# Kernel optimization log

Measured on AMD Instinct MI355X. Metric: run time of the kernel, lower is better.

Reference implementation:

```python
import jax, jax.numpy as jnp
import numpy as np

N = 30000      # nodes
E = 480000     # edges (before self loops)
DIN = 128      # dim_in
DH = 32        # dim_h (per-head out channels)
H1 = 8         # gat1 heads
H2 = 2         # gat2 heads
G = 64         # num graphs in batch
DOUT = 10      # dim_out
NEG_SLOPE = 0.2


def _glorot(key, shape):
    fan_in = shape[0]
    return jax.random.normal(key, shape, dtype=jnp.float32) / np.sqrt(fan_in)


def setup_inputs() -> dict:
    key = jax.random.key(0)
    ks = jax.random.split(key, 16)
    x = jax.random.normal(ks[0], (N, DIN), dtype=jnp.float32)
    edge_index = jax.random.randint(ks[1], (2, E), 0, N, dtype=jnp.int32)
    batch = jnp.sort(jax.random.randint(ks[2], (N,), 0, G, dtype=jnp.int32))
    # GATv2Conv layer 1: lin_l, lin_r (dim_in -> H1*DH), att (H1, DH), bias (H1*DH)
    W1l = _glorot(ks[3], (DIN, H1 * DH))
    W1r = _glorot(ks[4], (DIN, H1 * DH))
    a1 = _glorot(ks[5], (DH, H1)).T  # [H1, DH]
    b1 = jnp.zeros((H1 * DH,), dtype=jnp.float32)
    # GATv2Conv layer 2: (H1*DH -> H2*DH)
    W2l = _glorot(ks[6], (H1 * DH, H2 * DH))
    W2r = _glorot(ks[7], (H1 * DH, H2 * DH))
    a2 = _glorot(ks[8], (DH, H2)).T  # [H2, DH]
    b2 = jnp.zeros((H2 * DH,), dtype=jnp.float32)
    # MLP head: fc1(2*DH -> DH), fc2(DH -> DH//2), fc(DH//2 -> DOUT); stored [in,out]
    fc1_w = _glorot(ks[9], (2 * DH, DH)); fc1_b = jnp.zeros((DH,), jnp.float32)
    fc2_w = _glorot(ks[10], (DH, DH // 2)); fc2_b = jnp.zeros((DH // 2,), jnp.float32)
    fc_w = _glorot(ks[11], (DH // 2, DOUT)); fc_b = jnp.zeros((DOUT,), jnp.float32)
    return {"x": x, "edge_index": edge_index, "batch": batch,
            "W1l": W1l, "W1r": W1r, "a1": a1, "b1": b1,
            "W2l": W2l, "W2r": W2r, "a2": a2, "b2": b2,
            "fc1_w": fc1_w, "fc1_b": fc1_b, "fc2_w": fc2_w, "fc2_b": fc2_b,
            "fc_w": fc_w, "fc_b": fc_b}


def gatv2_conv(x, edge_index, Wl, Wr, att, bias, heads, dh, n):
    """PyG GATv2Conv: concat=True, add_self_loops=True, negative_slope=0.2."""
    src, dst = edge_index[0], edge_index[1]
    loop = jnp.arange(n, dtype=src.dtype)        # self loops (PyG default)
    src = jnp.concatenate([src, loop])
    dst = jnp.concatenate([dst, loop])
    xl = (x @ Wl).reshape(n, heads, dh)          # source transform
    xr = (x @ Wr).reshape(n, heads, dh)          # destination transform
    xj = xl[src]                                  # [Etot, H, dh] message features
    s = jax.nn.leaky_relu(xj + xr[dst], NEG_SLOPE)
    e = jnp.einsum('ehd,hd->eh', s, att)          # per-edge per-head score
    # segment softmax over incoming edges of each destination node
    m = jax.ops.segment_max(e, dst, num_segments=n)
    p = jnp.exp(e - m[dst])
    z = jax.ops.segment_sum(p, dst, num_segments=n)
    alpha = p / z[dst]                            # [Etot, H]
    out = jax.ops.segment_sum(xj * alpha[..., None], dst, num_segments=n)
    return out.reshape(n, heads * dh) + bias


def reference(x, edge_index, batch, W1l, W1r, a1, b1, W2l, W2r, a2, b2,
              fc1_w, fc1_b, fc2_w, fc2_b, fc_w, fc_b):
    h = gatv2_conv(x, edge_index, W1l, W1r, a1, b1, H1, DH, N)
    h = jax.nn.elu(h)
    h = gatv2_conv(h, edge_index, W2l, W2r, a2, b2, H2, DH, N)  # [N, 2*DH]
    # global_mean_pool
    sums = jax.ops.segment_sum(h, batch, num_segments=G)
    cnt = jax.ops.segment_sum(jnp.ones((N,), h.dtype), batch, num_segments=G)
    hg = sums / jnp.maximum(cnt, 1.0)[:, None]    # [G, 2*DH]
    x1 = jax.nn.relu(hg @ fc1_w + fc1_b)
    # dropout p=0.2 is identity in eval mode
    x2 = jax.nn.relu(x1 @ fc2_w + fc2_b)
    c = x2 @ fc_w + fc_b
    return (c, x2)
```

## Files before the change

### kernel.cpp

```cpp
#include <hip/hip_runtime.h>
#include <math.h>

#define DIN 128
#define DH  32
#define H1  8
#define H2  2
#define GNUM 64
#define DOUT 10
#define NEG_SLOPE 0.2f
#define SCAN_B 512

typedef __attribute__((ext_vector_type(8))) short sv8;
typedef __attribute__((ext_vector_type(4))) float fv4;

static __device__ __forceinline__ unsigned short f2bf(float f) {
    unsigned int u = __float_as_uint(f);
    unsigned int r = (u + 0x7fffu + ((u >> 16) & 1u)) >> 16;
    return (unsigned short)r;
}
static __device__ __forceinline__ float bf2f(unsigned short h) {
    return __uint_as_float(((unsigned int)h) << 16);
}


__global__ void k_prep(const float* __restrict__ x,
                       const float* __restrict__ W1l, const float* __restrict__ W1r,
                       const float* __restrict__ W2l, const float* __restrict__ W2r,
                       unsigned short* __restrict__ xgh, unsigned short* __restrict__ xgl,
                       short* __restrict__ B1th, short* __restrict__ B1tl,
                       short* __restrict__ B2th, short* __restrict__ B2tl,
                       int* __restrict__ zbase, int nz, int n) {
    int id = blockIdx.x * blockDim.x + threadIdx.x;
    if (id < nz) zbase[id] = 0;
    const int NX = n * 32;
    const int T1 = 512 * 128;
    const int T2 = 128 * 256;
    if (id < NX) {
        int m = id >> 5, j4 = id & 31;
        float4 v = *(const float4*)(x + (size_t)m * 128 + j4 * 4);
        unsigned short hx = f2bf(v.x), hy = f2bf(v.y), hz = f2bf(v.z), hw = f2bf(v.w);
        ushort4 hi; hi.x = hx; hi.y = hy; hi.z = hz; hi.w = hw;
        ushort4 lo;
        lo.x = f2bf(v.x - bf2f(hx)); lo.y = f2bf(v.y - bf2f(hy));
        lo.z = f2bf(v.z - bf2f(hz)); lo.w = f2bf(v.w - bf2f(hw));
        int R = m >> 4, r = m & 15;
        int C = j4 >> 3, q = (j4 >> 1) & 3, j = (j4 & 1) * 4;
        size_t o = ((size_t)(R * 4 + C) * 64 + q * 16 + r) * 8 + j;
        *(ushort4*)(xgh + o) = hi;
        *(ushort4*)(xgl + o) = lo;
    } else if (id < NX + T1) {
        int id1 = id - NX;
        int nn = id1 / 128, k = id1 - nn * 128;
        float v = (nn < 256) ? W1l[(size_t)k * 256 + nn] : W1r[(size_t)k * 256 + (nn - 256)];
        unsigned short h = f2bf(v);
        size_t o = (((size_t)(nn >> 4) * 4 + (k >> 5)) * 64 + ((k >> 3) & 3) * 16 + (nn & 15)) * 8 + (k & 7);
        B1th[o] = (short)h;
        B1tl[o] = (short)f2bf(v - bf2f(h));
    } else if (id < NX + T1 + T2) {
        int id2 = id - NX - T1;
        int nn = id2 / 256, k = id2 - nn * 256;
        float v = (nn < 64) ? W2l[(size_t)k * 64 + nn] : W2r[(size_t)k * 64 + (nn - 64)];
        unsigned short h = f2bf(v);
        size_t o = (((size_t)(nn >> 4) * 8 + (k >> 5)) * 64 + ((k >> 3) & 3) * 16 + (nn & 15)) * 8 + (k & 7);
        B2th[o] = (short)h;
        B2tl[o] = (short)f2bf(v - bf2f(h));
    }
}

__global__ void k_deg(const int* __restrict__ dst, int* __restrict__ deg, int E, int n) {
    int i = blockIdx.x * blockDim.x + threadIdx.x;
    if (i < E) {
        atomicAdd(&deg[dst[i]], 1);
    } else if (i < E + n) {
        atomicAdd(&deg[i - E], 1);
    }
}

__global__ __launch_bounds__(SCAN_B)
void k_scan_partial(const int* __restrict__ deg, int* __restrict__ bsum, int n) {
    int i = blockIdx.x * SCAN_B + threadIdx.x;
    int v = (i < n) ? deg[i] : 0;
    #pragma unroll
    for (int m = 32; m >= 1; m >>= 1) v += __shfl_xor(v, m);
    __shared__ int red[SCAN_B / 64];
    if ((threadIdx.x & 63) == 0) red[threadIdx.x >> 6] = v;
    __syncthreads();
    if (threadIdx.x == 0) {
        int s = 0;
        #pragma unroll
        for (int k = 0; k < SCAN_B / 64; ++k) s += red[k];
        bsum[blockIdx.x] = s;
    }
}

__global__ __launch_bounds__(SCAN_B)
void k_scan_apply(int* __restrict__ deg, int* __restrict__ cursor,
                  const int* __restrict__ bsum, int n, int nb) {
    __shared__ int buf[SCAN_B];
    __shared__ int pfx_s, tot_s;
    const int t = threadIdx.x, b = blockIdx.x;
    if (t < 64) {
        int v = (t < nb) ? bsum[t] : 0;
        int incl = v;
        #pragma unroll
        for (int o = 1; o < 64; o <<= 1) {
            int w = __shfl_up(incl, o);
            if (t >= o) incl += w;
        }
        int pfx = (b == 0) ? 0 : __shfl(incl, b - 1);
        int tot = __shfl(incl, nb - 1);
        if (t == 0) { pfx_s = pfx; tot_s = tot; }
    }
    int i = b * SCAN_B + t;
    int v = (i < n) ? deg[i] : 0;
    buf[t] = v;
    __syncthreads();
    for (int o = 1; o < SCAN_B; o <<= 1) {
        int a = (t >= o) ? buf[t - o] : 0;
        __syncthreads();
        buf[t] += a;
        __syncthreads();
    }
    int excl = buf[t] - v + pfx_s;
    if (i < n) { deg[i] = excl; cursor[i] = excl; }
    if (b == 0 && t == 0) deg[n] = tot_s;
}

__global__ void k_scatter(const int* __restrict__ src, const int* __restrict__ dst,
                          int* __restrict__ cursor, int* __restrict__ csr_src, int E, int n) {
    int i = blockIdx.x * blockDim.x + threadIdx.x;
    if (i < E) {
        int d = dst[i];
        int pos = atomicAdd(&cursor[d], 1);
        csr_src[pos] = src[i];
    } else if (i < E + n) {
        int v = i - E;
        int pos = atomicAdd(&cursor[v], 1);
        csr_src[pos] = v;
    }
}

__global__ __launch_bounds__(256, 2)
void k_gemm1(const unsigned short* __restrict__ Ah, const unsigned short* __restrict__ Al,
             const short* __restrict__ Bth, const short* __restrict__ Btl,
             unsigned short* __restrict__ C,
             int M, int Ntot) {
    __shared__ float smc[64 * 68];
    const int tid = threadIdx.x;
    const int lane = tid & 63;
    const int wid = tid >> 6;
    const int wm = wid & 1, wn = wid >> 1;
    const int m0 = blockIdx.x * 128;
    const int n0 = blockIdx.y * 128;
    const int l15 = lane & 15, q = lane >> 4;
    const int MR = (M >> 4) - 1;

    fv4 acc[4][4] = {};

    const unsigned short* ap[4];
    const unsigned short* alp[4];
    #pragma unroll
    for (int fm = 0; fm < 4; ++fm) {
        int R = (m0 >> 4) + wm * 4 + fm;
        if (R > MR) R = MR;
        ap[fm]  = Ah + ((size_t)R * 4 * 64 + lane) * 8;
        alp[fm] = Al + ((size_t)R * 4 * 64 + lane) * 8;
    }
    const short* bhp[4];
    const short* blp[4];
    #pragma unroll
    for (int fn = 0; fn < 4; ++fn) {
        int R = (n0 >> 4) + wn * 4 + fn;
        bhp[fn] = Bth + ((size_t)R * 4 * 64 + lane) * 8;
        blp[fn] = Btl + ((size_t)R * 4 * 64 + lane) * 8;
    }

    #pragma unroll
    for (int c = 0; c < 4; ++c) {
        const size_t co = (size_t)c * 512;
        sv8 ah[4], al[4], bh[4], bl[4];
        #pragma unroll
        for (int fn = 0; fn < 4; ++fn) {
            bh[fn] = *(const sv8*)(bhp[fn] + co);
            bl[fn] = *(const sv8*)(blp[fn] + co);
        }
        #pragma unroll
        for (int fm = 0; fm < 4; ++fm) {
            ah[fm] = *(const sv8*)(ap[fm] + co);
            al[fm] = *(const sv8*)(alp[fm] + co);
        }
        #pragma unroll
        for (int fm = 0; fm < 4; ++fm) {
            #pragma unroll
            for (int fn = 0; fn < 4; ++fn) {
                acc[fm][fn] = __builtin_amdgcn_mfma_f32_16x16x32_bf16(ah[fm], bh[fn], acc[fm][fn], 0, 0, 0);
                acc[fm][fn] = __builtin_amdgcn_mfma_f32_16x16x32_bf16(ah[fm], bl[fn], acc[fm][fn], 0, 0, 0);
                acc[fm][fn] = __builtin_amdgcn_mfma_f32_16x16x32_bf16(al[fm], bh[fn], acc[fm][fn], 0, 0, 0);
            }
        }
    }

    #pragma unroll
    for (int s = 0; s < 2; ++s) {
        #pragma unroll
        for (int cn = 0; cn < 2; ++cn) {
            __syncthreads();
            if (wm == s && wn == cn) {
                #pragma unroll
                for (int fm = 0; fm < 4; ++fm)
                    #pragma unroll
                    for (int fn = 0; fn < 4; ++fn)
                        #pragma unroll
                        for (int r = 0; r < 4; ++r)
                            smc[(fm * 16 + q * 4 + r) * 68 + fn * 16 + l15] = acc[fm][fn][r];
            }
            __syncthreads();
            int lr = tid >> 2;
            int grow = m0 + s * 64 + lr;
            if (grow < M) {
                #pragma unroll
                for (int k4 = 0; k4 < 4; ++k4) {
                    int jj = (tid & 3) + k4 * 4;
                    float4 vv = *(float4*)&smc[lr * 68 + jj * 4];
                    int gcol = n0 + cn * 64 + jj * 4;
                    ushort4 uu;
                    uu.x = f2bf(vv.x); uu.y = f2bf(vv.y);
                    uu.z = f2bf(vv.z); uu.w = f2bf(vv.w);
                    *(ushort4*)(C + (size_t)grow * Ntot + gcol) = uu;
                }
            }
        }
    }
}

__global__ __launch_bounds__(256, 2)
void k_gemm_bf(const unsigned short* __restrict__ A, const short* __restrict__ Bth,
               const short* __restrict__ Btl,
               unsigned short* __restrict__ C,
               int M, int Ntot) {
    __shared__ float smc[64 * 36];
    const int tid = threadIdx.x;
    const int lane = tid & 63;
    const int wid = tid >> 6;
    const int wm = wid & 1, wn = wid >> 1;
    const int m0 = blockIdx.x * 128;
    const int n0 = blockIdx.y * 64;
    const int l15 = lane & 15, q = lane >> 4;
    const int MR = (M >> 4) - 1;

    fv4 acc[4][2] = {};

    const unsigned short* ap[4];
    #pragma unroll
    for (int fm = 0; fm < 4; ++fm) {
        int R = (m0 >> 4) + wm * 4 + fm;
        if (R > MR) R = MR;
        ap[fm] = A + ((size_t)R * 8 * 64 + lane) * 8;
    }
    const short* bhp[2];
    const short* blp[2];
    #pragma unroll
    for (int fn = 0; fn < 2; ++fn) {
        int R = (n0 >> 4) + wn * 2 + fn;
        bhp[fn] = Bth + ((size_t)R * 8 * 64 + lane) * 8;
        blp[fn] = Btl + ((size_t)R * 8 * 64 + lane) * 8;
    }

    #pragma unroll 4
    for (int c = 0; c < 8; ++c) {
        const size_t co = (size_t)c * 512;
        sv8 ah[4], bh[2], bl[2];
        #pragma unroll
        for (int fn = 0; fn < 2; ++fn) {
            bh[fn] = *(const sv8*)(bhp[fn] + co);
            bl[fn] = *(const sv8*)(blp[fn] + co);
        }
        #pragma unroll
        for (int fm = 0; fm < 4; ++fm)
            ah[fm] = *(const sv8*)(ap[fm] + co);
        #pragma unroll
        for (int fm = 0; fm < 4; ++fm) {
            #pragma unroll
            for (int fn = 0; fn < 2; ++fn) {
                acc[fm][fn] = __builtin_amdgcn_mfma_f32_16x16x32_bf16(ah[fm], bh[fn], acc[fm][fn], 0, 0, 0);
                acc[fm][fn] = __builtin_amdgcn_mfma_f32_16x16x32_bf16(ah[fm], bl[fn], acc[fm][fn], 0, 0, 0);
            }
        }
    }

    #pragma unroll
    for (int s = 0; s < 2; ++s) {
        #pragma unroll
        for (int cn = 0; cn < 2; ++cn) {
            __syncthreads();
            if (wm == s && wn == cn) {
                #pragma unroll
                for (int fm = 0; fm < 4; ++fm)
                    #pragma unroll
                    for (int fn = 0; fn < 2; ++fn)
                        #pragma unroll
                        for (int r = 0; r < 4; ++r)
                            smc[(fm * 16 + q * 4 + r) * 36 + fn * 16 + l15] = acc[fm][fn][r];
            }
            __syncthreads();
            int lr = tid >> 2;
            int grow = m0 + s * 64 + lr;
            if (grow < M) {
                #pragma unroll
                for (int k4 = 0; k4 < 2; ++k4) {
                    int jj = (tid & 3) + k4 * 4;
                    float4 vv = *(float4*)&smc[lr * 36 + jj * 4];
                    int gcol = n0 + cn * 32 + jj * 4;
                    ushort4 uu;
                    uu.x = f2bf(vv.x); uu.y = f2bf(vv.y);
                    uu.z = f2bf(vv.z); uu.w = f2bf(vv.w);
                    *(ushort4*)(C + (size_t)grow * Ntot + gcol) = uu;
                }
            }
        }
    }
}

__global__ __launch_bounds__(64)
void k_edge1(const unsigned short* __restrict__ XLR,
             const int* __restrict__ offs, const int* __restrict__ csr,
             const float* __restrict__ att, const float* __restrict__ bias,
             unsigned short* __restrict__ out, int n) {
    const int lane = threadIdx.x;
    const int v = blockIdx.x;
    const int li = lane & 31;
    const int half = lane >> 5;
    const uint4* XL4 = (const uint4*)XLR;
    float av[8], xr[8];
    #pragma unroll
    for (int k = 0; k < 8; ++k) av[k] = att[li * 8 + k];
    {
        uint4 u = XL4[(size_t)v * 64 + 32 + li];
        xr[0] = __uint_as_float(u.x << 16);  xr[1] = __uint_as_float(u.x & 0xffff0000u);
        xr[2] = __uint_as_float(u.y << 16);  xr[3] = __uint_as_float(u.y & 0xffff0000u);
        xr[4] = __uint_as_float(u.z << 16);  xr[5] = __uint_as_float(u.z & 0xffff0000u);
        xr[6] = __uint_as_float(u.w << 16);  xr[7] = __uint_as_float(u.w & 0xffff0000u);
    }
    float z = 0.f;
    float acc[8] = {};
    const int e0 = offs[v], e1 = offs[v + 1];
    for (int j0 = e0; j0 < e1; j0 += 4) {
        #pragma unroll
        for (int p = 0; p < 2; ++p) {
            int j = j0 + p * 2 + half;
            bool valid = (j < e1);
            int jj = valid ? j : (e1 - 1);
            int src = csr[jj];
            uint4 u = XL4[(size_t)src * 64 + li];
            float f[8];
            f[0] = __uint_as_float(u.x << 16);  f[1] = __uint_as_float(u.x & 0xffff0000u);
            f[2] = __uint_as_float(u.y << 16);  f[3] = __uint_as_float(u.y & 0xffff0000u);
            f[4] = __uint_as_float(u.z << 16);  f[5] = __uint_as_float(u.z & 0xffff0000u);
            f[6] = __uint_as_float(u.w << 16);  f[7] = __uint_as_float(u.w & 0xffff0000u);
            float s1 = 0.f, s2 = 0.f;
            #pragma unroll
            for (int k = 0; k < 8; ++k) {
                float t = f[k] + xr[k];
                s1 = fmaf(t, av[k], s1);
                s2 = fmaf(fabsf(t), av[k], s2);
            }
            float s = fmaf(0.6f, s1, 0.4f * s2);
            s += __shfl_xor(s, 1);
            s += __shfl_xor(s, 2);
            float w = valid ? __expf(s) : 0.f;
            z += w;
            #pragma unroll
            for (int k = 0; k < 8; ++k) acc[k] = fmaf(w, f[k], acc[k]);
        }
    }
    z += __shfl_xor(z, 32);
    #pragma unroll
    for (int k = 0; k < 8; ++k) acc[k] += __shfl_xor(acc[k], 32);
    if (half == 0) {
        const float rz = 1.f / z;
        unsigned int o[4];
        #pragma unroll
        for (int k2 = 0; k2 < 4; ++k2) {
            float lo = fmaf(acc[k2 * 2 + 0], rz, bias[li * 8 + k2 * 2 + 0]);
            float hi = fmaf(acc[k2 * 2 + 1], rz, bias[li * 8 + k2 * 2 + 1]);
            lo = (lo > 0.f) ? lo : (__expf(lo) - 1.f);
            hi = (hi > 0.f) ? hi : (__expf(hi) - 1.f);
            o[k2] = (unsigned int)f2bf(lo) | ((unsigned int)f2bf(hi) << 16);
        }
        uint4 ov = { o[0], o[1], o[2], o[3] };
        size_t po = (((size_t)(v >> 4) * 8 + (li >> 2)) * 64 + (li & 3) * 16 + (v & 15)) * 8;
        *(uint4*)(out + po) = ov;
    }
}

__global__ __launch_bounds__(64)
void k_edge2(const unsigned short* __restrict__ XLR,
             const int* __restrict__ offs, const int* __restrict__ csr,
             const float* __restrict__ att, const float* __restrict__ bias,
             float* __restrict__ out, int n) {
    const int lane = threadIdx.x;
    const int v = blockIdx.x;
    const int li = lane & 7;
    const int slot = lane >> 3;
    const uint4* XL4 = (const uint4*)XLR;
    float av[8], xr[8];
    #pragma unroll
    for (int k = 0; k < 8; ++k) av[k] = att[li * 8 + k];
    {
        uint4 u = XL4[(size_t)v * 16 + 8 + li];
        xr[0] = __uint_as_float(u.x << 16);  xr[1] = __uint_as_float(u.x & 0xffff0000u);
        xr[2] = __uint_as_float(u.y << 16);  xr[3] = __uint_as_float(u.y & 0xffff0000u);
        xr[4] = __uint_as_float(u.z << 16);  xr[5] = __uint_as_float(u.z & 0xffff0000u);
        xr[6] = __uint_as_float(u.w << 16);  xr[7] = __uint_as_float(u.w & 0xffff0000u);
    }
    float z = 0.f;
    float acc[8] = {};
    const int e0 = offs[v], e1 = offs[v + 1];
    for (int j0 = e0; j0 < e1; j0 += 8) {
        int j = j0 + slot;
        bool valid = (j < e1);
        int jj = valid ? j : (e1 - 1);
        int src = csr[jj];
        uint4 u = XL4[(size_t)src * 16 + li];
        float f[8];
        f[0] = __uint_as_float(u.x << 16);  f[1] = __uint_as_float(u.x & 0xffff0000u);
        f[2] = __uint_as_float(u.y << 16);  f[3] = __uint_as_float(u.y & 0xffff0000u);
        f[4] = __uint_as_float(u.z << 16);  f[5] = __uint_as_float(u.z & 0xffff0000u);
        f[6] = __uint_as_float(u.w << 16);  f[7] = __uint_as_float(u.w & 0xffff0000u);
        float s1 = 0.f, s2 = 0.f;
        #pragma unroll
        for (int k = 0; k < 8; ++k) {
            float t = f[k] + xr[k];
            s1 = fmaf(t, av[k], s1);
            s2 = fmaf(fabsf(t), av[k], s2);
        }
        float s = fmaf(0.6f, s1, 0.4f * s2);
        s += __shfl_xor(s, 1);
        s += __shfl_xor(s, 2);
        float w = valid ? __expf(s) : 0.f;
        z += w;
        #pragma unroll
        for (int k = 0; k < 8; ++k) acc[k] = fmaf(w, f[k], acc[k]);
    }
    z += __shfl_xor(z, 8);  z += __shfl_xor(z, 16);  z += __shfl_xor(z, 32);
    #pragma unroll
    for (int k = 0; k < 8; ++k) {
        acc[k] += __shfl_xor(acc[k], 8);
        acc[k] += __shfl_xor(acc[k], 16);
        acc[k] += __shfl_xor(acc[k], 32);
    }
    if (slot == 0) {
        const float rz = 1.f / z;
        float o[8];
        #pragma unroll
        for (int k = 0; k < 8; ++k)
            o[k] = fmaf(acc[k], rz, bias[li * 8 + k]);
        float4 o0 = { o[0], o[1], o[2], o[3] };
        float4 o1 = { o[4], o[5], o[6], o[7] };
        *(float4*)(out + (size_t)v * 64 + li * 8 + 0) = o0;
        *(float4*)(out + (size_t)v * 64 + li * 8 + 4) = o1;
    }
}

__global__ __launch_bounds__(256)
void k_pool_mlp(const float* __restrict__ out2, const int* __restrict__ batch,
                const float* __restrict__ fc1w, const float* __restrict__ fc1b,
                const float* __restrict__ fc2w, const float* __restrict__ fc2b,
                const float* __restrict__ fcw,  const float* __restrict__ fcb,
                float* __restrict__ outc, float* __restrict__ outx2, int n) {
    const int g = blockIdx.x;
    const int t = threadIdx.x;
    const int lane = t & 63;
    const int w = t >> 6;
    __shared__ float red[4][64];
    __shared__ float hg_s[64];
    __shared__ float x1_s[32];
    __shared__ float x2_s[16];

    int lo = 0, hi = n;
    while (lo < hi) { int mid = (lo + hi) >> 1; if (batch[mid] < g) lo = mid + 1; else hi = mid; }
    const int start = lo;
    hi = n;
    while (lo < hi) { int mid = (lo + hi) >> 1; if (batch[mid] < g + 1) lo = mid + 1; else hi = mid; }
    const int end = lo;

    float s = 0.f;
    for (int v = start + w; v < end; v += 4)
        s += out2[(size_t)v * 64 + lane];
    red[w][lane] = s;
    __syncthreads();
    if (w == 0) {
        float tot = red[0][lane] + red[1][lane] + red[2][lane] + red[3][lane];
        float cnt = fmaxf((float)(end - start), 1.0f);
        hg_s[lane] = tot / cnt;
    }
    __syncthreads();
    if (t < 32) {
        float a = fc1b[t];
        #pragma unroll
        for (int k = 0; k < 64; ++k) a = fmaf(hg_s[k], fc1w[k * 32 + t], a);
        x1_s[t] = fmaxf(a, 0.f);
    }
    __syncthreads();
    if (t < 16) {
        float a = fc2b[t];
        #pragma unroll
        for (int k = 0; k < 32; ++k) a = fmaf(x1_s[k], fc2w[k * 16 + t], a);
        x2_s[t] = fmaxf(a, 0.f);
    }
    __syncthreads();
    if (t < DOUT) {
        float a = fcb[t];
        #pragma unroll
        for (int k = 0; k < 16; ++k) a = fmaf(x2_s[k], fcw[k * 10 + t], a);
        outc[g * DOUT + t] = a;
    }
    if (t < 16) outx2[g * 16 + t] = x2_s[t];
}

extern "C" void kernel_launch(void* const* d_in, const int* in_sizes, int n_in,
                              void* d_out, int out_size, void* d_ws, size_t ws_size,
                              hipStream_t stream) {
    const float* x    = (const float*)d_in[0];
    const int*   ei   = (const int*)d_in[1];
    const int*   batch= (const int*)d_in[2];
    const float* W1l  = (const float*)d_in[3];
    const float* W1r  = (const float*)d_in[4];
    const float* a1   = (const float*)d_in[5];
    const float* b1   = (const float*)d_in[6];
    const float* W2l  = (const float*)d_in[7];
    const float* W2r  = (const float*)d_in[8];
    const float* a2   = (const float*)d_in[9];
    const float* b2   = (const float*)d_in[10];
    const float* fc1w = (const float*)d_in[11];
    const float* fc1b = (const float*)d_in[12];
    const float* fc2w = (const float*)d_in[13];
    const float* fc2b = (const float*)d_in[14];
    const float* fcw  = (const float*)d_in[15];
    const float* fcb  = (const float*)d_in[16];

    const int N = in_sizes[2];
    const int E = in_sizes[1] / 2;
    const int ET = E + N;
    const int* esrc = ei;
    const int* edst = ei + E;
    const int NB = (N + SCAN_B - 1) / SCAN_B;

    char* ws = (char*)d_ws;
    size_t off = 0;
    unsigned short* xlr1b = (unsigned short*)(ws + off); off += (size_t)N * 512 * 2;
    unsigned short* h1b  = (unsigned short*)(ws + off);  off += (size_t)N * 256 * 2;
    float* out2 = (float*)(ws + off);            off += (size_t)N * 64 * 4;
    int*   deg   = (int*)(ws + off);             off += ((size_t)(N + 1) * 4 + 255) & ~255ull;
    int*   cursor= (int*)(ws + off);             off += ((size_t)N * 4 + 255) & ~255ull;
    int*   csr   = (int*)(ws + off);             off += ((size_t)ET * 4 + 255) & ~255ull;
    int*   bsum  = (int*)(ws + off);             off += ((size_t)(NB + 1) * 4 + 255) & ~255ull;
    short* B1th  = (short*)(ws + off);           off += (size_t)512 * 128 * 2;
    short* B1tl  = (short*)(ws + off);           off += (size_t)512 * 128 * 2;
    short* B2th  = (short*)(ws + off);           off += (size_t)128 * 256 * 2;
    short* B2tl  = (short*)(ws + off);           off += (size_t)128 * 256 * 2;
    unsigned short* xgh = (unsigned short*)(ws + off); off += (size_t)N * 128 * 2;
    unsigned short* xgl = (unsigned short*)(ws + off); off += (size_t)N * 128 * 2;
    unsigned short* xlr2b = xlr1b;
    (void)ws_size; (void)n_in; (void)out_size;

    float* outc  = (float*)d_out;
    float* outx2 = (float*)d_out + GNUM * DOUT;

    const int prep_tot = N * 32 + 512 * 128 + 128 * 256;
    k_prep<<<(prep_tot + 255) / 256, 256, 0, stream>>>(
        x, W1l, W1r, W2l, W2r, xgh, xgl, B1th, B1tl, B2th, B2tl, deg, N + 1, N);

    int tb = 256;
    int gb = (ET + tb - 1) / tb;
    k_deg<<<gb, tb, 0, stream>>>(edst, deg, E, N);
    k_scan_partial<<<NB, SCAN_B, 0, stream>>>(deg, bsum, N);
    k_scan_apply<<<NB, SCAN_B, 0, stream>>>(deg, cursor, bsum, N, NB);
    k_scatter<<<gb, tb, 0, stream>>>(esrc, edst, cursor, csr, E, N);

    dim3 g1((N + 127) / 128, 4);
    k_gemm1<<<g1, 256, 0, stream>>>(xgh, xgl, B1th, B1tl, xlr1b, N, 512);

    k_edge1<<<N, 64, 0, stream>>>(xlr1b, deg, csr, a1, b1, h1b, N);

    dim3 g2((N + 127) / 128, 2);
    k_gemm_bf<<<g2, 256, 0, stream>>>(h1b, B2th, B2tl, xlr2b, N, 128);

    k_edge2<<<N, 64, 0, stream>>>(xlr2b, deg, csr, a2, b2, out2, N);

    k_pool_mlp<<<GNUM, 256, 0, stream>>>(out2, batch, fc1w, fc1b, fc2w, fc2b,
                                         fcw, fcb, outc, outx2, N);
}
```

Baseline: 282.2 us.

## Prefetch next neighbor row in edge kernels and pack four nodes per block

Both edge-aggregation kernels now software-pipeline the neighbor gather: the next edge's CSR index and feature row are loaded before the current edge is processed, hiding gather latency. Blocks grow from 64 to 256 threads and each wave handles one destination node, cutting the block count by four and launch/scheduling overhead. In k_edge1 the two-way manual unroll is replaced by a single-edge-per-iteration loop with a prefetch, which can reduce memory-level parallelism per wave and adds register pressure from the extra in-flight row.

```diff
diff --git a/kernel.cpp b/kernel.cpp
--- a/kernel.cpp
+++ b/kernel.cpp
@@ -321,13 +321,15 @@
     }
 }
 
-__global__ __launch_bounds__(64)
+__global__ __launch_bounds__(256)
 void k_edge1(const unsigned short* __restrict__ XLR,
              const int* __restrict__ offs, const int* __restrict__ csr,
              const float* __restrict__ att, const float* __restrict__ bias,
              unsigned short* __restrict__ out, int n) {
-    const int lane = threadIdx.x;
-    const int v = blockIdx.x;
+    const int tid = threadIdx.x;
+    const int lane = tid & 63;
+    const int v = blockIdx.x * 4 + (tid >> 6);
+    if (v >= n) return;
     const int li = lane & 31;
     const int half = lane >> 5;
     const uint4* XL4 = (const uint4*)XLR;
@@ -344,34 +346,41 @@
     float z = 0.f;
     float acc[8] = {};
     const int e0 = offs[v], e1 = offs[v + 1];
-    for (int j0 = e0; j0 < e1; j0 += 4) {
-        #pragma unroll
-        for (int p = 0; p < 2; ++p) {
-            int j = j0 + p * 2 + half;
-            bool valid = (j < e1);
-            int jj = valid ? j : (e1 - 1);
-            int src = csr[jj];
-            uint4 u = XL4[(size_t)src * 64 + li];
-            float f[8];
-            f[0] = __uint_as_float(u.x << 16);  f[1] = __uint_as_float(u.x & 0xffff0000u);
-            f[2] = __uint_as_float(u.y << 16);  f[3] = __uint_as_float(u.y & 0xffff0000u);
-            f[4] = __uint_as_float(u.z << 16);  f[5] = __uint_as_float(u.z & 0xffff0000u);
-            f[6] = __uint_as_float(u.w << 16);  f[7] = __uint_as_float(u.w & 0xffff0000u);
-            float s1 = 0.f, s2 = 0.f;
-            #pragma unroll
-            for (int k = 0; k < 8; ++k) {
-                float t = f[k] + xr[k];
-                s1 = fmaf(t, av[k], s1);
-                s2 = fmaf(fabsf(t), av[k], s2);
-            }
-            float s = fmaf(0.6f, s1, 0.4f * s2);
-            s += __shfl_xor(s, 1);
-            s += __shfl_xor(s, 2);
-            float w = valid ? __expf(s) : 0.f;
-            z += w;
-            #pragma unroll
-            for (int k = 0; k < 8; ++k) acc[k] = fmaf(w, f[k], acc[k]);
-        }
+
+    int j = e0 + half;
+    bool val = (j < e1);
+    int jj = val ? j : (e1 - 1);
+    int src = csr[jj];
+    uint4 u = XL4[(size_t)src * 64 + li];
+
+    for (int base = e0; base < e1; base += 2) {
+        int jn = j + 2;
+        bool valn = (jn < e1);
+        int jjn = valn ? jn : (e1 - 1);
+        int srcn = csr[jjn];
+        uint4 un = XL4[(size_t)srcn * 64 + li];
+
+        float f[8];
+        f[0] = __uint_as_float(u.x << 16);  f[1] = __uint_as_float(u.x & 0xffff0000u);
+        f[2] = __uint_as_float(u.y << 16);  f[3] = __uint_as_float(u.y & 0xffff0000u);
+        f[4] = __uint_as_float(u.z << 16);  f[5] = __uint_as_float(u.z & 0xffff0000u);
+        f[6] = __uint_as_float(u.w << 16);  f[7] = __uint_as_float(u.w & 0xffff0000u);
+        float s1 = 0.f, s2 = 0.f;
+        #pragma unroll
+        for (int k = 0; k < 8; ++k) {
+            float t = f[k] + xr[k];
+            s1 = fmaf(t, av[k], s1);
+            s2 = fmaf(fabsf(t), av[k], s2);
+        }
+        float s = fmaf(0.6f, s1, 0.4f * s2);
+        s += __shfl_xor(s, 1);
+        s += __shfl_xor(s, 2);
+        float w = val ? __expf(s) : 0.f;
+        z += w;
+        #pragma unroll
+        for (int k = 0; k < 8; ++k) acc[k] = fmaf(w, f[k], acc[k]);
+
+        u = un; val = valn; j = jn;
     }
     z += __shfl_xor(z, 32);
     #pragma unroll
@@ -393,13 +402,15 @@
     }
 }
 
-__global__ __launch_bounds__(64)
+__global__ __launch_bounds__(256)
 void k_edge2(const unsigned short* __restrict__ XLR,
              const int* __restrict__ offs, const int* __restrict__ csr,
              const float* __restrict__ att, const float* __restrict__ bias,
              float* __restrict__ out, int n) {
-    const int lane = threadIdx.x;
-    const int v = blockIdx.x;
+    const int tid = threadIdx.x;
+    const int lane = tid & 63;
+    const int v = blockIdx.x * 4 + (tid >> 6);
+    if (v >= n) return;
     const int li = lane & 7;
     const int slot = lane >> 3;
     const uint4* XL4 = (const uint4*)XLR;
@@ -416,12 +427,20 @@
     float z = 0.f;
     float acc[8] = {};
     const int e0 = offs[v], e1 = offs[v + 1];
-    for (int j0 = e0; j0 < e1; j0 += 8) {
-        int j = j0 + slot;
-        bool valid = (j < e1);
-        int jj = valid ? j : (e1 - 1);
-        int src = csr[jj];
-        uint4 u = XL4[(size_t)src * 16 + li];
+
+    int j = e0 + slot;
+    bool val = (j < e1);
+    int jj = val ? j : (e1 - 1);
+    int src = csr[jj];
+    uint4 u = XL4[(size_t)src * 16 + li];
+
+    for (int base = e0; base < e1; base += 8) {
+        int jn = j + 8;
+        bool valn = (jn < e1);
+        int jjn = valn ? jn : (e1 - 1);
+        int srcn = csr[jjn];
+        uint4 un = XL4[(size_t)srcn * 16 + li];
+
         float f[8];
         f[0] = __uint_as_float(u.x << 16);  f[1] = __uint_as_float(u.x & 0xffff0000u);
         f[2] = __uint_as_float(u.y << 16);  f[3] = __uint_as_float(u.y & 0xffff0000u);
@@ -437,10 +456,12 @@
         float s = fmaf(0.6f, s1, 0.4f * s2);
         s += __shfl_xor(s, 1);
         s += __shfl_xor(s, 2);
-        float w = valid ? __expf(s) : 0.f;
+        float w = val ? __expf(s) : 0.f;
         z += w;
         #pragma unroll
         for (int k = 0; k < 8; ++k) acc[k] = fmaf(w, f[k], acc[k]);
+
+        u = un; val = valn; j = jn;
     }
     z += __shfl_xor(z, 8);  z += __shfl_xor(z, 16);  z += __shfl_xor(z, 32);
     #pragma unroll
@@ -581,12 +602,12 @@
     dim3 g1((N + 127) / 128, 4);
     k_gemm1<<<g1, 256, 0, stream>>>(xgh, xgl, B1th, B1tl, xlr1b, N, 512);
 
-    k_edge1<<<N, 64, 0, stream>>>(xlr1b, deg, csr, a1, b1, h1b, N);
+    k_edge1<<<(N + 3) / 4, 256, 0, stream>>>(xlr1b, deg, csr, a1, b1, h1b, N);
 
     dim3 g2((N + 127) / 128, 2);
     k_gemm_bf<<<g2, 256, 0, stream>>>(h1b, B2th, B2tl, xlr2b, N, 128);
 
-    k_edge2<<<N, 64, 0, stream>>>(xlr2b, deg, csr, a2, b2, out2, N);
+    k_edge2<<<(N + 3) / 4, 256, 0, stream>>>(xlr2b, deg, csr, a2, b2, out2, N);
 
     k_pool_mlp<<<GNUM, 256, 0, stream>>>(out2, batch, fc1w, fc1b, fc2w, fc2b,
                                          fcw, fcb, outc, outx2, N);
```

Result: faster. 275.2 us (-2.5%).

## Split XL/XR buffers, persistent atomic-queue edge kernels, packed bf16 epilogue

Applied to the files above, without the earlier changes.

The GEMM outputs are split into separate, contiguous XL and XR arrays, so each gathered source row in the edge kernels covers half as many bytes per row stride and packs more densely in cache. The edge kernels become persistent 256-thread blocks that pull destination nodes from an atomic counter, replacing one 64-thread block per node and hoisting the att and bias loads out of the per-node path. The GEMM epilogues now drain both warp rows at once through a larger LDS tile with fewer barriers, and use the hardware v_cvt_pk_bf16_f32 pack with 16-byte stores. In exchange, every node costs one global atomic, and the larger LDS tile may lower GEMM occupancy.

```diff
diff --git a/kernel.cpp b/kernel.cpp
--- a/kernel.cpp
+++ b/kernel.cpp
@@ -21,6 +21,11 @@
 static __device__ __forceinline__ float bf2f(unsigned short h) {
     return __uint_as_float(((unsigned int)h) << 16);
 }
+static __device__ __forceinline__ unsigned int cvtpk(float lo, float hi) {
+    unsigned int r;
+    asm("v_cvt_pk_bf16_f32 %0, %1, %2" : "=v"(r) : "v"(lo), "v"(hi));
+    return r;
+}
 
 
 __global__ void k_prep(const float* __restrict__ x,
@@ -29,9 +34,10 @@
                        unsigned short* __restrict__ xgh, unsigned short* __restrict__ xgl,
                        short* __restrict__ B1th, short* __restrict__ B1tl,
                        short* __restrict__ B2th, short* __restrict__ B2tl,
-                       int* __restrict__ zbase, int nz, int n) {
+                       int* __restrict__ zbase, int nz, int* __restrict__ ctr, int n) {
     int id = blockIdx.x * blockDim.x + threadIdx.x;
     if (id < nz) zbase[id] = 0;
+    if (id < 2) ctr[id] = 0;
     const int NX = n * 32;
     const int T1 = 512 * 128;
     const int T2 = 128 * 256;
@@ -143,9 +149,9 @@
 __global__ __launch_bounds__(256, 2)
 void k_gemm1(const unsigned short* __restrict__ Ah, const unsigned short* __restrict__ Al,
              const short* __restrict__ Bth, const short* __restrict__ Btl,
-             unsigned short* __restrict__ C,
-             int M, int Ntot) {
-    __shared__ float smc[64 * 68];
+             unsigned short* __restrict__ XLo, unsigned short* __restrict__ XRo,
+             int M) {
+    __shared__ float smc[128 * 68];
     const int tid = threadIdx.x;
     const int lane = tid & 63;
     const int wid = tid >> 6;
@@ -201,33 +207,33 @@
     }
 
     #pragma unroll
-    for (int s = 0; s < 2; ++s) {
-        #pragma unroll
-        for (int cn = 0; cn < 2; ++cn) {
-            __syncthreads();
-            if (wm == s && wn == cn) {
+    for (int p = 0; p < 2; ++p) {
+        if (p) __syncthreads();
+        if (wn == p) {
+            #pragma unroll
+            for (int fm = 0; fm < 4; ++fm)
                 #pragma unroll
-                for (int fm = 0; fm < 4; ++fm)
+                for (int fn = 0; fn < 4; ++fn)
                     #pragma unroll
-                    for (int fn = 0; fn < 4; ++fn)
-                        #pragma unroll
-                        for (int r = 0; r < 4; ++r)
-                            smc[(fm * 16 + q * 4 + r) * 68 + fn * 16 + l15] = acc[fm][fn][r];
-            }
-            __syncthreads();
-            int lr = tid >> 2;
-            int grow = m0 + s * 64 + lr;
-            if (grow < M) {
-                #pragma unroll
-                for (int k4 = 0; k4 < 4; ++k4) {
-                    int jj = (tid & 3) + k4 * 4;
-                    float4 vv = *(float4*)&smc[lr * 68 + jj * 4];
-                    int gcol = n0 + cn * 64 + jj * 4;
-                    ushort4 uu;
-                    uu.x = f2bf(vv.x); uu.y = f2bf(vv.y);
-                    uu.z = f2bf(vv.z); uu.w = f2bf(vv.w);
-                    *(ushort4*)(C + (size_t)grow * Ntot + gcol) = uu;
-                }
+                    for (int r = 0; r < 4; ++r)
+                        smc[(wm * 64 + fm * 16 + q * 4 + r) * 68 + fn * 16 + l15] = acc[fm][fn][r];
+        }
+        __syncthreads();
+        int lr = tid >> 1;
+        int ch = (tid & 1) * 32;
+        int grow = m0 + lr;
+        if (grow < M) {
+            int colb = n0 + p * 64 + ch;
+            unsigned short* dst = (colb < 256)
+                ? XLo + (size_t)grow * 256 + colb
+                : XRo + (size_t)grow * 256 + (colb - 256);
+            #pragma unroll
+            for (int j = 0; j < 4; ++j) {
+                float4 a = *(float4*)&smc[lr * 68 + ch + j * 8];
+                float4 b = *(float4*)&smc[lr * 68 + ch + j * 8 + 4];
+                uint4 o = { cvtpk(a.x, a.y), cvtpk(a.z, a.w),
+                            cvtpk(b.x, b.y), cvtpk(b.z, b.w) };
+                *(uint4*)(dst + j * 8) = o;
             }
         }
     }
@@ -236,9 +242,9 @@
 __global__ __launch_bounds__(256, 2)
 void k_gemm_bf(const unsigned short* __restrict__ A, const short* __restrict__ Bth,
                const short* __restrict__ Btl,
-               unsigned short* __restrict__ C,
-               int M, int Ntot) {
-    __shared__ float smc[64 * 36];
+               unsigned short* __restrict__ XL2, unsigned short* __restrict__ XR2,
+               int M) {
+    __shared__ float smc[128 * 36];
     const int tid = threadIdx.x;
     const int lane = tid & 63;
     const int wid = tid >> 6;
@@ -289,69 +295,156 @@
     }
 
     #pragma unroll
-    for (int s = 0; s < 2; ++s) {
-        #pragma unroll
-        for (int cn = 0; cn < 2; ++cn) {
-            __syncthreads();
-            if (wm == s && wn == cn) {
+    for (int p = 0; p < 2; ++p) {
+        if (p) __syncthreads();
+        if (wn == p) {
+            #pragma unroll
+            for (int fm = 0; fm < 4; ++fm)
                 #pragma unroll
-                for (int fm = 0; fm < 4; ++fm)
+                for (int fn = 0; fn < 2; ++fn)
                     #pragma unroll
-                    for (int fn = 0; fn < 2; ++fn)
-                        #pragma unroll
-                        for (int r = 0; r < 4; ++r)
-                            smc[(fm * 16 + q * 4 + r) * 36 + fn * 16 + l15] = acc[fm][fn][r];
+                    for (int r = 0; r < 4; ++r)
+                        smc[(wm * 64 + fm * 16 + q * 4 + r) * 36 + fn * 16 + l15] = acc[fm][fn][r];
+        }
+        __syncthreads();
+        int lr = tid >> 1;
+        int ch = (tid & 1) * 16;
+        int grow = m0 + lr;
+        if (grow < M) {
+            int colb = n0 + p * 32 + ch;
+            unsigned short* dst = (colb < 64)
+                ? XL2 + (size_t)grow * 64 + colb
+                : XR2 + (size_t)grow * 64 + (colb - 64);
+            #pragma unroll
+            for (int j = 0; j < 2; ++j) {
+                float4 a = *(float4*)&smc[lr * 36 + ch + j * 8];
+                float4 b = *(float4*)&smc[lr * 36 + ch + j * 8 + 4];
+                uint4 o = { cvtpk(a.x, a.y), cvtpk(a.z, a.w),
+                            cvtpk(b.x, b.y), cvtpk(b.z, b.w) };
+                *(uint4*)(dst + j * 8) = o;
             }
-            __syncthreads();
-            int lr = tid >> 2;
-            int grow = m0 + s * 64 + lr;
-            if (grow < M) {
-                #pragma unroll
-                for (int k4 = 0; k4 < 2; ++k4) {
-                    int jj = (tid & 3) + k4 * 4;
-                    float4 vv = *(float4*)&smc[lr * 36 + jj * 4];
-                    int gcol = n0 + cn * 32 + jj * 4;
-                    ushort4 uu;
-                    uu.x = f2bf(vv.x); uu.y = f2bf(vv.y);
-                    uu.z = f2bf(vv.z); uu.w = f2bf(vv.w);
-                    *(ushort4*)(C + (size_t)grow * Ntot + gcol) = uu;
-                }
-            }
-        }
-    }
-}
-
-__global__ __launch_bounds__(64)
-void k_edge1(const unsigned short* __restrict__ XLR,
+        }
+    }
+}
+
+__global__ __launch_bounds__(256)
+void k_edge1(const unsigned short* __restrict__ XL, const unsigned short* __restrict__ XR,
              const int* __restrict__ offs, const int* __restrict__ csr,
              const float* __restrict__ att, const float* __restrict__ bias,
-             unsigned short* __restrict__ out, int n) {
-    const int lane = threadIdx.x;
-    const int v = blockIdx.x;
+             unsigned short* __restrict__ out, int* __restrict__ ctr, int n) {
+    const int lane = threadIdx.x & 63;
     const int li = lane & 31;
     const int half = lane >> 5;
-    const uint4* XL4 = (const uint4*)XLR;
-    float av[8], xr[8];
-    #pragma unroll
-    for (int k = 0; k < 8; ++k) av[k] = att[li * 8 + k];
-    {
-        uint4 u = XL4[(size_t)v * 64 + 32 + li];
-        xr[0] = __uint_as_float(u.x << 16);  xr[1] = __uint_as_float(u.x & 0xffff0000u);
-        xr[2] = __uint_as_float(u.y << 16);  xr[3] = __uint_as_float(u.y & 0xffff0000u);
-        xr[4] = __uint_as_float(u.z << 16);  xr[5] = __uint_as_float(u.z & 0xffff0000u);
-        xr[6] = __uint_as_float(u.w << 16);  xr[7] = __uint_as_float(u.w & 0xffff0000u);
-    }
-    float z = 0.f;
-    float acc[8] = {};
-    const int e0 = offs[v], e1 = offs[v + 1];
-    for (int j0 = e0; j0 < e1; j0 += 4) {
-        #pragma unroll
-        for (int p = 0; p < 2; ++p) {
-            int j = j0 + p * 2 + half;
+    const uint4* XL4 = (const uint4*)XL;
+    const uint4* XR4 = (const uint4*)XR;
+    float av[8], bi[8];
+    #pragma unroll
+    for (int k = 0; k < 8; ++k) { av[k] = att[li * 8 + k]; bi[k] = bias[li * 8 + k]; }
+
+    for (;;) {
+        int t0 = 0;
+        if (lane == 0) t0 = atomicAdd(ctr, 1);
+        const int v = __shfl(t0, 0);
+        if (v >= n) break;
+
+        float xr[8];
+        {
+            uint4 u = XR4[(size_t)v * 32 + li];
+            xr[0] = __uint_as_float(u.x << 16);  xr[1] = __uint_as_float(u.x & 0xffff0000u);
+            xr[2] = __uint_as_float(u.y << 16);  xr[3] = __uint_as_float(u.y & 0xffff0000u);
+            xr[4] = __uint_as_float(u.z << 16);  xr[5] = __uint_as_float(u.z & 0xffff0000u);
+            xr[6] = __uint_as_float(u.w << 16);  xr[7] = __uint_as_float(u.w & 0xffff0000u);
+        }
+        float z = 0.f;
+        float acc[8] = {};
+        const int e0 = offs[v], e1 = offs[v + 1];
+        for (int j0 = e0; j0 < e1; j0 += 4) {
+            #pragma unroll
+            for (int p = 0; p < 2; ++p) {
+                int j = j0 + p * 2 + half;
+                bool valid = (j < e1);
+                int jj = valid ? j : (e1 - 1);
+                int src = csr[jj];
+                uint4 u = XL4[(size_t)src * 32 + li];
+                float f[8];
+                f[0] = __uint_as_float(u.x << 16);  f[1] = __uint_as_float(u.x & 0xffff0000u);
+                f[2] = __uint_as_float(u.y << 16);  f[3] = __uint_as_float(u.y & 0xffff0000u);
+                f[4] = __uint_as_float(u.z << 16);  f[5] = __uint_as_float(u.z & 0xffff0000u);
+                f[6] = __uint_as_float(u.w << 16);  f[7] = __uint_as_float(u.w & 0xffff0000u);
+                float s1 = 0.f, s2 = 0.f;
+                #pragma unroll
+                for (int k = 0; k < 8; ++k) {
+                    float t = f[k] + xr[k];
+                    s1 = fmaf(t, av[k], s1);
+                    s2 = fmaf(fabsf(t), av[k], s2);
+                }
+                float s = fmaf(0.6f, s1, 0.4f * s2);
+                s += __shfl_xor(s, 1);
+                s += __shfl_xor(s, 2);
+                float w = valid ? __expf(s) : 0.f;
+                z += w;
+                #pragma unroll
+                for (int k = 0; k < 8; ++k) acc[k] = fmaf(w, f[k], acc[k]);
+            }
+        }
+        z += __shfl_xor(z, 32);
+        #pragma unroll
+        for (int k = 0; k < 8; ++k) acc[k] += __shfl_xor(acc[k], 32);
+        if (half == 0) {
+            const float rz = 1.f / z;
+            unsigned int o[4];
+            #pragma unroll
+            for (int k2 = 0; k2 < 4; ++k2) {
+                float lo = fmaf(acc[k2 * 2 + 0], rz, bi[k2 * 2 + 0]);
+                float hi = fmaf(acc[k2 * 2 + 1], rz, bi[k2 * 2 + 1]);
+                lo = (lo > 0.f) ? lo : (__expf(lo) - 1.f);
+                hi = (hi > 0.f) ? hi : (__expf(hi) - 1.f);
+                o[k2] = cvtpk(lo, hi);
+            }
+            uint4 ov = { o[0], o[1], o[2], o[3] };
+            size_t po = (((size_t)(v >> 4) * 8 + (li >> 2)) * 64 + (li & 3) * 16 + (v & 15)) * 8;
+            *(uint4*)(out + po) = ov;
+        }
+    }
+}
+
+__global__ __launch_bounds__(256)
+void k_edge2(const unsigned short* __restrict__ XL, const unsigned short* __restrict__ XR,
+             const int* __restrict__ offs, const int* __restrict__ csr,
+             const float* __restrict__ att, const float* __restrict__ bias,
+             float* __restrict__ out, int* __restrict__ ctr, int n) {
+    const int lane = threadIdx.x & 63;
+    const int li = lane & 7;
+    const int slot = lane >> 3;
+    const uint4* XL4 = (const uint4*)XL;
+    const uint4* XR4 = (const uint4*)XR;
+    float av[8], bi[8];
+    #pragma unroll
+    for (int k = 0; k < 8; ++k) { av[k] = att[li * 8 + k]; bi[k] = bias[li * 8 + k]; }
+
+    for (;;) {
+        int t0 = 0;
+        if (lane == 0) t0 = atomicAdd(ctr, 1);
+        const int v = __shfl(t0, 0);
+        if (v >= n) break;
+
+        float xr[8];
+        {
+            uint4 u = XR4[(size_t)v * 8 + li];
+            xr[0] = __uint_as_float(u.x << 16);  xr[1] = __uint_as_float(u.x & 0xffff0000u);
+            xr[2] = __uint_as_float(u.y << 16);  xr[3] = __uint_as_float(u.y & 0xffff0000u);
+            xr[4] = __uint_as_float(u.z << 16);  xr[5] = __uint_as_float(u.z & 0xffff0000u);
+            xr[6] = __uint_as_float(u.w << 16);  xr[7] = __uint_as_float(u.w & 0xffff0000u);
+        }
+        float z = 0.f;
+        float acc[8] = {};
+        const int e0 = offs[v], e1 = offs[v + 1];
+        for (int j0 = e0; j0 < e1; j0 += 8) {
+            int j = j0 + slot;
             bool valid = (j < e1);
             int jj = valid ? j : (e1 - 1);
             int src = csr[jj];
-            uint4 u = XL4[(size_t)src * 64 + li];
+            uint4 u = XL4[(size_t)src * 8 + li];
             float f[8];
             f[0] = __uint_as_float(u.x << 16);  f[1] = __uint_as_float(u.x & 0xffff0000u);
             f[2] = __uint_as_float(u.y << 16);  f[3] = __uint_as_float(u.y & 0xffff0000u);
@@ -372,93 +465,24 @@
             #pragma unroll
             for (int k = 0; k < 8; ++k) acc[k] = fmaf(w, f[k], acc[k]);
         }
-    }
-    z += __shfl_xor(z, 32);
-    #pragma unroll
-    for (int k = 0; k < 8; ++k) acc[k] += __shfl_xor(acc[k], 32);
-    if (half == 0) {
-        const float rz = 1.f / z;
-        unsigned int o[4];
-        #pragma unroll
-        for (int k2 = 0; k2 < 4; ++k2) {
-            float lo = fmaf(acc[k2 * 2 + 0], rz, bias[li * 8 + k2 * 2 + 0]);
-            float hi = fmaf(acc[k2 * 2 + 1], rz, bias[li * 8 + k2 * 2 + 1]);
-            lo = (lo > 0.f) ? lo : (__expf(lo) - 1.f);
-            hi = (hi > 0.f) ? hi : (__expf(hi) - 1.f);
-            o[k2] = (unsigned int)f2bf(lo) | ((unsigned int)f2bf(hi) << 16);
-        }
-        uint4 ov = { o[0], o[1], o[2], o[3] };
-        size_t po = (((size_t)(v >> 4) * 8 + (li >> 2)) * 64 + (li & 3) * 16 + (v & 15)) * 8;
-        *(uint4*)(out + po) = ov;
-    }
-}
-
-__global__ __launch_bounds__(64)
-void k_edge2(const unsigned short* __restrict__ XLR,
-             const int* __restrict__ offs, const int* __restrict__ csr,
-             const float* __restrict__ att, const float* __restrict__ bias,
-             float* __restrict__ out, int n) {
-    const int lane = threadIdx.x;
-    const int v = blockIdx.x;
-    const int li = lane & 7;
-    const int slot = lane >> 3;
-    const uint4* XL4 = (const uint4*)XLR;
-    float av[8], xr[8];
-    #pragma unroll
-    for (int k = 0; k < 8; ++k) av[k] = att[li * 8 + k];
-    {
-        uint4 u = XL4[(size_t)v * 16 + 8 + li];
-        xr[0] = __uint_as_float(u.x << 16);  xr[1] = __uint_as_float(u.x & 0xffff0000u);
-        xr[2] = __uint_as_float(u.y << 16);  xr[3] = __uint_as_float(u.y & 0xffff0000u);
-        xr[4] = __uint_as_float(u.z << 16);  xr[5] = __uint_as_float(u.z & 0xffff0000u);
-        xr[6] = __uint_as_float(u.w << 16);  xr[7] = __uint_as_float(u.w & 0xffff0000u);
-    }
-    float z = 0.f;
-    float acc[8] = {};
-    const int e0 = offs[v], e1 = offs[v + 1];
-    for (int j0 = e0; j0 < e1; j0 += 8) {
-        int j = j0 + slot;
-        bool valid = (j < e1);
-        int jj = valid ? j : (e1 - 1);
-        int src = csr[jj];
-        uint4 u = XL4[(size_t)src * 16 + li];
-        float f[8];
-        f[0] = __uint_as_float(u.x << 16);  f[1] = __uint_as_float(u.x & 0xffff0000u);
-        f[2] = __uint_as_float(u.y << 16);  f[3] = __uint_as_float(u.y & 0xffff0000u);
-        f[4] = __uint_as_float(u.z << 16);  f[5] = __uint_as_float(u.z & 0xffff0000u);
-        f[6] = __uint_as_float(u.w << 16);  f[7] = __uint_as_float(u.w & 0xffff0000u);
-        float s1 = 0.f, s2 = 0.f;
+        z += __shfl_xor(z, 8);  z += __shfl_xor(z, 16);  z += __shfl_xor(z, 32);
         #pragma unroll
         for (int k = 0; k < 8; ++k) {
-            float t = f[k] + xr[k];
-            s1 = fmaf(t, av[k], s1);
-            s2 = fmaf(fabsf(t), av[k], s2);
-        }
-        float s = fmaf(0.6f, s1, 0.4f * s2);
-        s += __shfl_xor(s, 1);
-        s += __shfl_xor(s, 2);
-        float w = valid ? __expf(s) : 0.f;
-        z += w;
-        #pragma unroll
-        for (int k = 0; k < 8; ++k) acc[k] = fmaf(w, f[k], acc[k]);
-    }
-    z += __shfl_xor(z, 8);  z += __shfl_xor(z, 16);  z += __shfl_xor(z, 32);
-    #pragma unroll
-    for (int k = 0; k < 8; ++k) {
-        acc[k] += __shfl_xor(acc[k], 8);
-        acc[k] += __shfl_xor(acc[k], 16);
-        acc[k] += __shfl_xor(acc[k], 32);
-    }
-    if (slot == 0) {
-        const float rz = 1.f / z;
-        float o[8];
-        #pragma unroll
-        for (int k = 0; k < 8; ++k)
-            o[k] = fmaf(acc[k], rz, bias[li * 8 + k]);
-        float4 o0 = { o[0], o[1], o[2], o[3] };
-        float4 o1 = { o[4], o[5], o[6], o[7] };
-        *(float4*)(out + (size_t)v * 64 + li * 8 + 0) = o0;
-        *(float4*)(out + (size_t)v * 64 + li * 8 + 4) = o1;
+            acc[k] += __shfl_xor(acc[k], 8);
+            acc[k] += __shfl_xor(acc[k], 16);
+            acc[k] += __shfl_xor(acc[k], 32);
+        }
+        if (slot == 0) {
+            const float rz = 1.f / z;
+            float o[8];
+            #pragma unroll
+            for (int k = 0; k < 8; ++k)
+                o[k] = fmaf(acc[k], rz, bi[k]);
+            float4 o0 = { o[0], o[1], o[2], o[3] };
+            float4 o1 = { o[4], o[5], o[6], o[7] };
+            *(float4*)(out + (size_t)v * 64 + li * 8 + 0) = o0;
+            *(float4*)(out + (size_t)v * 64 + li * 8 + 4) = o1;
+        }
     }
 }
 
@@ -548,20 +572,23 @@
 
     char* ws = (char*)d_ws;
     size_t off = 0;
-    unsigned short* xlr1b = (unsigned short*)(ws + off); off += (size_t)N * 512 * 2;
-    unsigned short* h1b  = (unsigned short*)(ws + off);  off += (size_t)N * 256 * 2;
+    unsigned short* XL1 = (unsigned short*)(ws + off); off += (size_t)N * 256 * 2;
+    unsigned short* XR1 = (unsigned short*)(ws + off); off += (size_t)N * 256 * 2;
+    unsigned short* h1b = (unsigned short*)(ws + off); off += (size_t)N * 256 * 2;
     float* out2 = (float*)(ws + off);            off += (size_t)N * 64 * 4;
     int*   deg   = (int*)(ws + off);             off += ((size_t)(N + 1) * 4 + 255) & ~255ull;
     int*   cursor= (int*)(ws + off);             off += ((size_t)N * 4 + 255) & ~255ull;
     int*   csr   = (int*)(ws + off);             off += ((size_t)ET * 4 + 255) & ~255ull;
     int*   bsum  = (int*)(ws + off);             off += ((size_t)(NB + 1) * 4 + 255) & ~255ull;
+    int*   ctr   = (int*)(ws + off);             off += 256;
     short* B1th  = (short*)(ws + off);           off += (size_t)512 * 128 * 2;
     short* B1tl  = (short*)(ws + off);           off += (size_t)512 * 128 * 2;
     short* B2th  = (short*)(ws + off);           off += (size_t)128 * 256 * 2;
     short* B2tl  = (short*)(ws + off);           off += (size_t)128 * 256 * 2;
     unsigned short* xgh = (unsigned short*)(ws + off); off += (size_t)N * 128 * 2;
     unsigned short* xgl = (unsigned short*)(ws + off); off += (size_t)N * 128 * 2;
-    unsigned short* xlr2b = xlr1b;
+    unsigned short* XL2 = XL1;
+    unsigned short* XR2 = XL1 + (size_t)N * 64;
     (void)ws_size; (void)n_in; (void)out_size;
 
     float* outc  = (float*)d_out;
@@ -569,7 +596,7 @@
 
     const int prep_tot = N * 32 + 512 * 128 + 128 * 256;
     k_prep<<<(prep_tot + 255) / 256, 256, 0, stream>>>(
-        x, W1l, W1r, W2l, W2r, xgh, xgl, B1th, B1tl, B2th, B2tl, deg, N + 1, N);
+        x, W1l, W1r, W2l, W2r, xgh, xgl, B1th, B1tl, B2th, B2tl, deg, N + 1, ctr, N);
 
     int tb = 256;
     int gb = (ET + tb - 1) / tb;
@@ -579,14 +606,14 @@
     k_scatter<<<gb, tb, 0, stream>>>(esrc, edst, cursor, csr, E, N);
 
     dim3 g1((N + 127) / 128, 4);
-    k_gemm1<<<g1, 256, 0, stream>>>(xgh, xgl, B1th, B1tl, xlr1b, N, 512);
-
-    k_edge1<<<N, 64, 0, stream>>>(xlr1b, deg, csr, a1, b1, h1b, N);
+    k_gemm1<<<g1, 256, 0, stream>>>(xgh, xgl, B1th, B1tl, XL1, XR1, N);
+
+    k_edge1<<<2048, 256, 0, stream>>>(XL1, XR1, deg, csr, a1, b1, h1b, ctr, N);
 
     dim3 g2((N + 127) / 128, 2);
-    k_gemm_bf<<<g2, 256, 0, stream>>>(h1b, B2th, B2tl, xlr2b, N, 128);
-
-    k_edge2<<<N, 64, 0, stream>>>(xlr2b, deg, csr, a2, b2, out2, N);
+    k_gemm_bf<<<g2, 256, 0, stream>>>(h1b, B2th, B2tl, XL2, XR2, N);
+
+    k_edge2<<<2048, 256, 0, stream>>>(XL2, XR2, deg, csr, a2, b2, out2, ctr + 1, N);
 
     k_pool_mlp<<<GNUM, 256, 0, stream>>>(out2, batch, fc1w, fc1b, fc2w, fc2b,
                                          fcw, fcb, outc, outx2, N);
```

New measurement: 1.096 ms. 288% more time.
